# Optimization experiments

Measured on AMD Instinct MI355X. Metric: run time of the kernel, lower is better.

Reference implementation:

```python
import jax, jax.numpy as jnp
import numpy as np

N_NODES = 100000
C = 128
E = 800000
V = 50000
NEG_SLOPE = 0.2


def gat_conv(x, edges, W, att_src, att_dst, bias, num_nodes):
    """Single-head PyG-style GATConv with self-loops added (PyG default).

    edges: [2, E] with row 0 = source j, row 1 = destination i.
    """
    loops = jnp.arange(num_nodes, dtype=edges.dtype)
    src = jnp.concatenate([edges[0], loops])  # [E+N]
    dst = jnp.concatenate([edges[1], loops])

    h = x @ W.T                               # [N, C] linear transform
    a_s = h @ att_src                         # [N] per-node src score
    a_d = h @ att_dst                         # [N] per-node dst score

    e = jax.nn.leaky_relu(a_s[src] + a_d[dst], NEG_SLOPE)  # [E+N]
    # scatter-softmax over edges grouped by destination node
    m = jax.ops.segment_max(e, dst, num_segments=num_nodes)
    ex = jnp.exp(e - m[dst])
    denom = jax.ops.segment_sum(ex, dst, num_segments=num_nodes)
    alpha = ex / (denom[dst] + 1e-16)         # [E+N]

    out = jax.ops.segment_sum(alpha[:, None] * h[src], dst, num_segments=num_nodes)
    return out + bias


def setup_inputs() -> dict:
    key = jax.random.key(0)
    ks = jax.random.split(key, 12)
    s = 1.0 / np.sqrt(C)
    return {
        "embedding": jax.random.normal(ks[0], (N_NODES, C), jnp.float32),
        "W1": jax.random.normal(ks[1], (C, C), jnp.float32) * s,
        "att_src1": jax.random.normal(ks[2], (C,), jnp.float32) * s,
        "att_dst1": jax.random.normal(ks[3], (C,), jnp.float32) * s,
        "b1": jax.random.normal(ks[4], (C,), jnp.float32) * s,
        "W2": jax.random.normal(ks[5], (C, C), jnp.float32) * s,
        "att_src2": jax.random.normal(ks[6], (C,), jnp.float32) * s,
        "att_dst2": jax.random.normal(ks[7], (C,), jnp.float32) * s,
        "b2": jax.random.normal(ks[8], (C,), jnp.float32) * s,
        "edges1": jax.random.randint(ks[9], (2, E), 0, N_NODES, jnp.int64 if jax.config.jax_enable_x64 else jnp.int32),
        "edges2": jax.random.randint(ks[10], (2, E), 0, N_NODES, jnp.int64 if jax.config.jax_enable_x64 else jnp.int32),
        "idx_mapping": jax.random.randint(ks[11], (V,), 0, N_NODES, jnp.int64 if jax.config.jax_enable_x64 else jnp.int32),
    }


def reference(embedding, W1, att_src1, att_dst1, b1, W2, att_src2, att_dst2, b2,
              edges1, edges2, idx_mapping):
    h = gat_conv(embedding, edges1, W1, att_src1, att_dst1, b1, N_NODES)
    h = gat_conv(h, edges2, W2, att_src2, att_dst2, b2, N_NODES)
    return h[idx_mapping]
```

## Files before the change

kernel.cpp:

```cpp
#include <hip/hip_runtime.h>

#define N_NODES 100000
#define C_DIM 128
#define E_EDGES 800000
#define V_OUT 50000
#define EN (E_EDGES + N_NODES)
#define M2 (2 * N_NODES)
#define EN2 (2 * EN)

#define BSHIFT 9
#define NBUCK_L ((N_NODES + 511) >> 9)
#define NBUCK2 (2 * NBUCK_L)
#define CAP 8192
#define P1_CHUNK 4096
#define P1_PER_T (P1_CHUNK / 256)
#define NCHUNK ((EN2 + P1_CHUNK - 1) / P1_CHUNK)

#define XPAD 136

typedef unsigned int uint;
typedef unsigned short ushort;
typedef __attribute__((ext_vector_type(8))) short bf16x8;
typedef __attribute__((ext_vector_type(4))) float f32x4;

static __device__ __forceinline__ ushort f2bf(float f) {
    uint u = __float_as_uint(f);
    u += 0x7fffu + ((u >> 16) & 1);
    return (ushort)(u >> 16);
}

__global__ void f2bf_kernel(const float* __restrict__ in, ushort* __restrict__ out, int n4)
{
    int i = blockIdx.x * 256 + threadIdx.x;
    if (i >= n4) return;
    float4 v = reinterpret_cast<const float4*>(in)[i];
    ushort4 r;
    r.x = f2bf(v.x); r.y = f2bf(v.y); r.z = f2bf(v.z); r.w = f2bf(v.w);
    reinterpret_cast<ushort4*>(out)[i] = r;
}

__global__ void vflag_kernel(const int* __restrict__ idx, int* __restrict__ vflag)
{
    int v = blockIdx.x * 256 + threadIdx.x;
    if (v < V_OUT) vflag[idx[v]] = 1;
}

template <int IN_F32>
__global__ __launch_bounds__(256) void gemm_mfma(
    const void* __restrict__ xin, const ushort* __restrict__ Wb,
    const float* __restrict__ att_s, const float* __restrict__ att_d,
    ushort* __restrict__ hb, float* __restrict__ a_s, float* __restrict__ a_d)
{
    __shared__ ushort xs[64 * XPAD];
    __shared__ ushort ws[128 * XPAD];
    const int tid = threadIdx.x;
    const int nb = blockIdx.x * 64;

    {
        const int row = tid >> 2, q = tid & 3;
        const long srow = min(nb + row, N_NODES - 1);
        ushort* dst = &xs[row * XPAD + q * 32];
        if (IN_F32) {
            const float* src = (const float*)xin + srow * 128 + q * 32;
            #pragma unroll
            for (int i = 0; i < 4; ++i) {
                float4 u = *reinterpret_cast<const float4*>(src + i * 8);
                float4 v = *reinterpret_cast<const float4*>(src + i * 8 + 4);
                uint4 pk;
                pk.x = (uint)f2bf(u.x) | ((uint)f2bf(u.y) << 16);
                pk.y = (uint)f2bf(u.z) | ((uint)f2bf(u.w) << 16);
                pk.z = (uint)f2bf(v.x) | ((uint)f2bf(v.y) << 16);
                pk.w = (uint)f2bf(v.z) | ((uint)f2bf(v.w) << 16);
                *reinterpret_cast<uint4*>(dst + i * 8) = pk;
            }
        } else {
            const ushort* src = (const ushort*)xin + srow * 128 + q * 32;
            #pragma unroll
            for (int i = 0; i < 4; ++i)
                *reinterpret_cast<uint4*>(dst + i * 8) =
                    *reinterpret_cast<const uint4*>(src + i * 8);
        }
    }
    {
        const int row = tid >> 1, half = tid & 1;
        const ushort* src = Wb + row * 128 + half * 64;
        ushort* dst = &ws[row * XPAD + half * 64];
        #pragma unroll
        for (int i = 0; i < 8; ++i)
            *reinterpret_cast<uint4*>(dst + i * 8) =
                *reinterpret_cast<const uint4*>(src + i * 8);
    }
    __syncthreads();

    const int lane = tid & 63;
    const int wv   = tid >> 6;
    const int n0   = nb + wv * 16;
    if (n0 >= N_NODES) return;
    const int m    = lane & 15;
    const int quad = lane >> 4;

    bf16x8 a[4];
    #pragma unroll
    for (int ki = 0; ki < 4; ++ki)
        a[ki] = *reinterpret_cast<const bf16x8*>(&xs[(wv * 16 + m) * XPAD + quad * 8 + ki * 32]);

    float ps[4] = {0, 0, 0, 0}, pd[4] = {0, 0, 0, 0};

    #pragma unroll
    for (int ct = 0; ct < 8; ++ct) {
        const int c = ct * 16 + m;
        f32x4 acc = {0.f, 0.f, 0.f, 0.f};
        #pragma unroll
        for (int ki = 0; ki < 4; ++ki) {
            bf16x8 b = *reinterpret_cast<const bf16x8*>(&ws[c * XPAD + quad * 8 + ki * 32]);
            acc = __builtin_amdgcn_mfma_f32_16x16x32_bf16(a[ki], b, acc, 0, 0, 0);
        }
        const float asc = att_s[c], adc = att_d[c];
        #pragma unroll
        for (int r = 0; r < 4; ++r) {
            const int node = n0 + quad * 4 + r;
            hb[(long)node * 128 + c] = f2bf(acc[r]);
            ps[r] = fmaf(acc[r], asc, ps[r]);
            pd[r] = fmaf(acc[r], adc, pd[r]);
        }
    }
    #pragma unroll
    for (int r = 0; r < 4; ++r) {
        float s = ps[r], d = pd[r];
        #pragma unroll
        for (int x = 1; x < 16; x <<= 1) { s += __shfl_xor(s, x); d += __shfl_xor(d, x); }
        if (m == 0) {
            const int node = n0 + quad * 4 + r;
            a_s[node] = s; a_d[node] = d;
        }
    }
}

__global__ __launch_bounds__(256) void partition_kernel(
    const int* __restrict__ e1, const int* __restrict__ e2,
    int* __restrict__ cursor, uint* __restrict__ slab)
{
    __shared__ int cnt[NBUCK2];
    __shared__ int basearr[NBUCK2];
    const int tid = threadIdx.x;
    for (int i = tid; i < NBUCK2; i += 256) cnt[i] = 0;
    __syncthreads();

    const int e0 = blockIdx.x * P1_CHUNK;
    uint ent[P1_PER_T];
    int  bkt[P1_PER_T];
    #pragma unroll
    for (int i = 0; i < P1_PER_T; ++i) {
        int e = e0 + i * 256 + tid;
        bkt[i] = -1;
        if (e < EN2) {
            int src, dst, lb;
            if (e < EN) {
                if (e < E_EDGES) { src = e1[e]; dst = e1[E_EDGES + e]; }
                else             { src = dst = e - E_EDGES; }
                lb = 0;
            } else {
                int f = e - EN;
                if (f < E_EDGES) { src = e2[f]; dst = e2[E_EDGES + f]; }
                else             { src = dst = f - E_EDGES; }
                lb = NBUCK_L;
            }
            bkt[i] = lb + (dst >> BSHIFT);
            ent[i] = (uint)src | ((uint)(dst & 511) << 17);
            atomicAdd(&cnt[bkt[i]], 1);
        }
    }
    __syncthreads();
    for (int b = tid; b < NBUCK2; b += 256) {
        int c = cnt[b];
        basearr[b] = (c > 0) ? atomicAdd(&cursor[b], c) : 0;
        cnt[b] = 0;
    }
    __syncthreads();
    #pragma unroll
    for (int i = 0; i < P1_PER_T; ++i) {
        if (bkt[i] >= 0) {
            int r = basearr[bkt[i]] + atomicAdd(&cnt[bkt[i]], 1);
            if (r < CAP) slab[(long)bkt[i] * CAP + r] = ent[i];
        }
    }
}

__global__ void bucket_scan(const int* __restrict__ cursor, int* __restrict__ bbase)
{
    const int lane = threadIdx.x;
    int v[7]; int s = 0;
    #pragma unroll
    for (int i = 0; i < 7; ++i) {
        int idx = lane * 7 + i;
        v[i] = (idx < NBUCK2) ? cursor[idx] : 0;
        s += v[i];
    }
    int incl = s;
    #pragma unroll
    for (int d = 1; d < 64; d <<= 1) {
        int t = __shfl_up(incl, d);
        if (lane >= d) incl += t;
    }
    int excl = incl - s;
    #pragma unroll
    for (int i = 0; i < 7; ++i) {
        int idx = lane * 7 + i;
        if (idx < NBUCK2) bbase[idx] = excl;
        excl += v[i];
    }
}

__global__ __launch_bounds__(256) void local_csr(
    const uint* __restrict__ slab, const int* __restrict__ cursor,
    const int* __restrict__ bbase, int* __restrict__ offs, uint* __restrict__ esrc)
{
    __shared__ uint ent[CAP];
    __shared__ int deg[512];
    __shared__ int excl[512];
    const int b = blockIdx.x;
    const int tid = threadIdx.x;
    const int cnt = min(cursor[b], CAP);
    const int base = bbase[b];
    const int layer = (b >= NBUCK_L);
    const int node0 = (b - layer * NBUCK_L) << BSHIFT;
    const int obase = layer * N_NODES;
    const int nodes_n = min(512, N_NODES - node0);

    for (int i = tid; i < 512; i += 256) deg[i] = 0;
    __syncthreads();
    for (int i = tid; i < cnt; i += 256) {
        uint v = slab[(long)b * CAP + i];
        ent[i] = v;
        atomicAdd(&deg[v >> 17], 1);
    }
    __syncthreads();
    if (tid < 64) {
        int v8[8]; int s = 0;
        #pragma unroll
        for (int i = 0; i < 8; ++i) { v8[i] = deg[tid * 8 + i]; s += v8[i]; }
        int incl = s;
        #pragma unroll
        for (int d = 1; d < 64; d <<= 1) {
            int t = __shfl_up(incl, d);
            if (tid >= d) incl += t;
        }
        int e = incl - s;
        #pragma unroll
        for (int i = 0; i < 8; ++i) { excl[tid * 8 + i] = e; e += v8[i]; }
    }
    __syncthreads();
    for (int i = tid; i < nodes_n; i += 256)
        offs[obase + node0 + i] = base + excl[i];
    for (int i = tid; i < 512; i += 256) deg[i] = 0;
    if (tid == 0 && node0 + 512 >= N_NODES)
        offs[obase + N_NODES] = base + cnt;
    __syncthreads();
    for (int i = tid; i < cnt; i += 256) {
        uint v = ent[i];
        int dl = v >> 17;
        int r = atomicAdd(&deg[dl], 1);
        esrc[base + excl[dl] + r] = v;
    }
}

__global__ __launch_bounds__(256) void weights_kernel(
    const float* __restrict__ a_s, const float* __restrict__ a_d,
    const uint* __restrict__ esrc, const int* __restrict__ cursor,
    const int* __restrict__ bbase, float* __restrict__ wv, int bucket0)
{
    const int b = bucket0 + (blockIdx.x >> 2);
    const int cnt = min(cursor[b], CAP);
    const int base = bbase[b];
    const int node0 = (b - bucket0) << BSHIFT;
    for (int i = (blockIdx.x & 3) * 256 + threadIdx.x; i < cnt; i += 1024) {
        uint v = esrc[base + i];
        float e = a_s[v & 0x1ffff] + a_d[node0 + (v >> 17)];
        e = (e >= 0.0f) ? e : 0.2f * e;
        wv[base + i] = __expf(e);
    }
}

template <int MODE>
__global__ __launch_bounds__(256) void aggregate(
    const ushort* __restrict__ hb, const float* __restrict__ wv,
    const float* __restrict__ bias,
    const int* __restrict__ offs, const uint* __restrict__ esrc,
    const int* __restrict__ vflag, void* __restrict__ outp, int obase)
{
    const int wave = threadIdx.x >> 6;
    const int lane = threadIdx.x & 63;
    const int slot = lane >> 4;
    const int c16  = lane & 15;
    const int node = (blockIdx.x * 4 + wave) * 4 + slot;

    int start = offs[obase + node];
    int end   = offs[obase + node + 1];
    bool active = true;
    if (MODE == 1) { active = (vflag[node] != 0); if (!active) end = start; }

    const long coff = (long)(c16 << 3);
    float acc[8] = {0, 0, 0, 0, 0, 0, 0, 0};
    float dsum = 0.0f;

    if (start < end) {
        const int e1 = end - 1;
        uint v1 = 0; float w0, w1; uint4 h0;
        {
            uint v0 = esrc[start];
            w0 = wv[start];
            int jc = min(start + 1, e1);
            v1 = esrc[jc];
            w1 = (start + 1 < end) ? wv[jc] : 0.0f;
            h0 = *reinterpret_cast<const uint4*>(hb + ((long)(v0 & 0x1ffff) << 7) + coff);
        }
        for (int j = start; j < end; ++j) {
            const int j2 = j + 2;
            const int jc = min(j2, e1);
            uint  v2 = esrc[jc];
            float w2 = (j2 < end) ? wv[jc] : 0.0f;
            uint4 h1 = *reinterpret_cast<const uint4*>(hb + ((long)(v1 & 0x1ffff) << 7) + coff);
            dsum += w0;
            acc[0] = fmaf(w0, __uint_as_float(h0.x << 16),         acc[0]);
            acc[1] = fmaf(w0, __uint_as_float(h0.x & 0xffff0000u), acc[1]);
            acc[2] = fmaf(w0, __uint_as_float(h0.y << 16),         acc[2]);
            acc[3] = fmaf(w0, __uint_as_float(h0.y & 0xffff0000u), acc[3]);
            acc[4] = fmaf(w0, __uint_as_float(h0.z << 16),         acc[4]);
            acc[5] = fmaf(w0, __uint_as_float(h0.z & 0xffff0000u), acc[5]);
            acc[6] = fmaf(w0, __uint_as_float(h0.w << 16),         acc[6]);
            acc[7] = fmaf(w0, __uint_as_float(h0.w & 0xffff0000u), acc[7]);
            w0 = w1; h0 = h1; v1 = v2; w1 = w2;
        }
    }

    if (MODE == 1 && !active) return;

    const float inv = 1.0f / (dsum + 1e-16f);
    const int c0 = c16 << 3;
    const float4 b0 = *reinterpret_cast<const float4*>(bias + c0);
    const float4 b1 = *reinterpret_cast<const float4*>(bias + c0 + 4);
    float res[8];
    res[0] = fmaf(acc[0], inv, b0.x);
    res[1] = fmaf(acc[1], inv, b0.y);
    res[2] = fmaf(acc[2], inv, b0.z);
    res[3] = fmaf(acc[3], inv, b0.w);
    res[4] = fmaf(acc[4], inv, b1.x);
    res[5] = fmaf(acc[5], inv, b1.y);
    res[6] = fmaf(acc[6], inv, b1.z);
    res[7] = fmaf(acc[7], inv, b1.w);
    if (MODE == 0) {
        uint4 pk;
        pk.x = (uint)f2bf(res[0]) | ((uint)f2bf(res[1]) << 16);
        pk.y = (uint)f2bf(res[2]) | ((uint)f2bf(res[3]) << 16);
        pk.z = (uint)f2bf(res[4]) | ((uint)f2bf(res[5]) << 16);
        pk.w = (uint)f2bf(res[6]) | ((uint)f2bf(res[7]) << 16);
        *reinterpret_cast<uint4*>((ushort*)outp + ((long)node << 7) + c0) = pk;
    } else {
        float* op = (float*)outp + ((long)node << 7) + c0;
        *reinterpret_cast<float4*>(op)     = make_float4(res[0], res[1], res[2], res[3]);
        *reinterpret_cast<float4*>(op + 4) = make_float4(res[4], res[5], res[6], res[7]);
    }
}

__global__ void gather_out(const float* __restrict__ h, const int* __restrict__ idx,
                           float* __restrict__ out)
{
    int g = blockIdx.x * 256 + threadIdx.x;
    int v = g >> 5, c4 = (g & 31) << 2;
    long src = (long)idx[v] * C_DIM + c4;
    *reinterpret_cast<float4*>(out + ((long)v * C_DIM + c4)) =
        *reinterpret_cast<const float4*>(h + src);
}

extern "C" void kernel_launch(void* const* d_in, const int* in_sizes, int n_in,
                              void* d_out, int out_size, void* d_ws, size_t ws_size,
                              hipStream_t stream)
{
    const float* emb = (const float*)d_in[0];
    const float* W1  = (const float*)d_in[1];
    const float* as1 = (const float*)d_in[2];
    const float* ad1 = (const float*)d_in[3];
    const float* b1  = (const float*)d_in[4];
    const float* W2  = (const float*)d_in[5];
    const float* as2 = (const float*)d_in[6];
    const float* ad2 = (const float*)d_in[7];
    const float* b2  = (const float*)d_in[8];
    const int* edges1 = (const int*)d_in[9];
    const int* edges2 = (const int*)d_in[10];
    const int* idxm   = (const int*)d_in[11];
    float* out = (float*)d_out;

    char* p = (char*)d_ws;
    auto alloc = [&](size_t bytes) {
        char* r = p;
        p += (bytes + 255) & ~(size_t)255;
        return r;
    };
    float*  hB   = (float*)alloc((size_t)N_NODES * C_DIM * 4);
    ushort* hb   = (ushort*)alloc((size_t)N_NODES * C_DIM * 2);
    ushort* a1o  = (ushort*)alloc((size_t)N_NODES * C_DIM * 2);
    uint*   slab = (uint*)alloc((size_t)NBUCK2 * CAP * 4);
    uint*   esrc = (uint*)alloc((size_t)EN2 * 4);
    float*  wvb  = (float*)alloc((size_t)EN2 * 4);
    int*    offs = (int*)alloc((size_t)(M2 + 1) * 4);
    ushort* W1b  = (ushort*)alloc((size_t)C_DIM * C_DIM * 2);
    ushort* W2b  = (ushort*)alloc((size_t)C_DIM * C_DIM * 2);
    float*  aS   = (float*)alloc((size_t)N_NODES * 4);
    float*  aD   = (float*)alloc((size_t)N_NODES * 4);
    int*  bbase  = (int*)alloc((size_t)NBUCK2 * 4);
    int*  cursor = (int*)alloc((size_t)NBUCK2 * 4);
    int*  vflag  = (int*)alloc((size_t)N_NODES * 4);

    hipMemsetAsync(cursor, 0, (size_t)((char*)vflag - (char*)cursor) + (size_t)N_NODES * 4, stream);
    f2bf_kernel<<<(C_DIM * C_DIM / 4 + 255) / 256, 256, 0, stream>>>(W1, W1b, C_DIM * C_DIM / 4);
    f2bf_kernel<<<(C_DIM * C_DIM / 4 + 255) / 256, 256, 0, stream>>>(W2, W2b, C_DIM * C_DIM / 4);
    vflag_kernel<<<(V_OUT + 255) / 256, 256, 0, stream>>>(idxm, vflag);

    partition_kernel<<<NCHUNK, 256, 0, stream>>>(edges1, edges2, cursor, slab);
    bucket_scan<<<1, 64, 0, stream>>>(cursor, bbase);
    local_csr<<<NBUCK2, 256, 0, stream>>>(slab, cursor, bbase, offs, esrc);

    gemm_mfma<1><<<(N_NODES + 63) / 64, 256, 0, stream>>>(emb, W1b, as1, ad1, hb, aS, aD);
    weights_kernel<<<NBUCK_L * 4, 256, 0, stream>>>(aS, aD, esrc, cursor, bbase, wvb, 0);
    aggregate<0><<<N_NODES / 16, 256, 0, stream>>>(hb, wvb, b1, offs, esrc, vflag, a1o, 0);

    gemm_mfma<0><<<(N_NODES + 63) / 64, 256, 0, stream>>>(a1o, W2b, as2, ad2, hb, aS, aD);
    weights_kernel<<<NBUCK_L * 4, 256, 0, stream>>>(aS, aD, esrc, cursor, bbase, wvb, NBUCK_L);
    aggregate<1><<<N_NODES / 16, 256, 0, stream>>>(hb, wvb, b2, offs, esrc, vflag, hB, N_NODES);

    gather_out<<<(V_OUT * 32) / 256, 256, 0, stream>>>(hB, idxm, out);
}
```

Before: 288.2 us.

## Fuse edge weight computation into aggregation and merge prep kernels

Removes the separate weights kernel and its wv buffer. Each aggregation lane now gathers a_s[src] and a_d[node] and computes the leaky-relu exponent inline, with a deeper software pipeline so the a_s and h loads are prefetched two edges ahead. The three small prep launches (two weight conversions and the vflag marking) are merged into one kernel. This saves a full write and read of the per-edge weight array plus three launches, but every one of the 16 lanes per node now recomputes the same exp and does extra scattered a_s loads.

After: 284.1 us. Within noise of the previous version (-1.4%).

```diff
diff --git a/kernel.cpp b/kernel.cpp
--- a/kernel.cpp
+++ b/kernel.cpp
@@ -29,20 +29,25 @@
     return (ushort)(u >> 16);
 }
 
-__global__ void f2bf_kernel(const float* __restrict__ in, ushort* __restrict__ out, int n4)
-{
-    int i = blockIdx.x * 256 + threadIdx.x;
-    if (i >= n4) return;
-    float4 v = reinterpret_cast<const float4*>(in)[i];
-    ushort4 r;
-    r.x = f2bf(v.x); r.y = f2bf(v.y); r.z = f2bf(v.z); r.w = f2bf(v.w);
-    reinterpret_cast<ushort4*>(out)[i] = r;
-}
-
-__global__ void vflag_kernel(const int* __restrict__ idx, int* __restrict__ vflag)
-{
-    int v = blockIdx.x * 256 + threadIdx.x;
-    if (v < V_OUT) vflag[idx[v]] = 1;
+#define PREP_WBLK (C_DIM * C_DIM / 4 / 256)
+#define PREP_VBLK ((V_OUT + 255) / 256)
+__global__ void prep_kernel(const float* __restrict__ W1, const float* __restrict__ W2,
+                            ushort* __restrict__ W1b, ushort* __restrict__ W2b,
+                            const int* __restrict__ idx, int* __restrict__ vflag)
+{
+    const int b = blockIdx.x;
+    if (b < 2 * PREP_WBLK) {
+        const float* in  = (b < PREP_WBLK) ? W1 : W2;
+        ushort* outp     = (b < PREP_WBLK) ? W1b : W2b;
+        int i = (b % PREP_WBLK) * 256 + threadIdx.x;
+        float4 v = reinterpret_cast<const float4*>(in)[i];
+        ushort4 r;
+        r.x = f2bf(v.x); r.y = f2bf(v.y); r.z = f2bf(v.z); r.w = f2bf(v.w);
+        reinterpret_cast<ushort4*>(outp)[i] = r;
+    } else {
+        int v = (b - 2 * PREP_WBLK) * 256 + threadIdx.x;
+        if (v < V_OUT) vflag[idx[v]] = 1;
+    }
 }
 
 template <int IN_F32>
@@ -264,27 +269,10 @@
     }
 }
 
-__global__ __launch_bounds__(256) void weights_kernel(
-    const float* __restrict__ a_s, const float* __restrict__ a_d,
-    const uint* __restrict__ esrc, const int* __restrict__ cursor,
-    const int* __restrict__ bbase, float* __restrict__ wv, int bucket0)
-{
-    const int b = bucket0 + (blockIdx.x >> 2);
-    const int cnt = min(cursor[b], CAP);
-    const int base = bbase[b];
-    const int node0 = (b - bucket0) << BSHIFT;
-    for (int i = (blockIdx.x & 3) * 256 + threadIdx.x; i < cnt; i += 1024) {
-        uint v = esrc[base + i];
-        float e = a_s[v & 0x1ffff] + a_d[node0 + (v >> 17)];
-        e = (e >= 0.0f) ? e : 0.2f * e;
-        wv[base + i] = __expf(e);
-    }
-}
-
 template <int MODE>
 __global__ __launch_bounds__(256) void aggregate(
-    const ushort* __restrict__ hb, const float* __restrict__ wv,
-    const float* __restrict__ bias,
+    const ushort* __restrict__ hb, const float* __restrict__ a_s,
+    const float* __restrict__ a_d, const float* __restrict__ bias,
     const int* __restrict__ offs, const uint* __restrict__ esrc,
     const int* __restrict__ vflag, void* __restrict__ outp, int obase)
 {
@@ -304,22 +292,28 @@
     float dsum = 0.0f;
 
     if (start < end) {
+        const float ad = a_d[node];
         const int e1 = end - 1;
-        uint v1 = 0; float w0, w1; uint4 h0;
+        uint v0 = esrc[start];
+        uint v1 = esrc[min(start + 1, e1)];
+        uint v2 = esrc[min(start + 2, e1)];
+        float as1 = a_s[v1 & 0x1ffff];
+        uint4 h0 = *reinterpret_cast<const uint4*>(hb + ((long)(v0 & 0x1ffff) << 7) + coff);
+        uint4 h1 = *reinterpret_cast<const uint4*>(hb + ((long)(v1 & 0x1ffff) << 7) + coff);
+        float w0;
         {
-            uint v0 = esrc[start];
-            w0 = wv[start];
-            int jc = min(start + 1, e1);
-            v1 = esrc[jc];
-            w1 = (start + 1 < end) ? wv[jc] : 0.0f;
-            h0 = *reinterpret_cast<const uint4*>(hb + ((long)(v0 & 0x1ffff) << 7) + coff);
+            float e = a_s[v0 & 0x1ffff] + ad;
+            e = (e >= 0.0f) ? e : 0.2f * e;
+            w0 = __expf(e);
         }
         for (int j = start; j < end; ++j) {
-            const int j2 = j + 2;
-            const int jc = min(j2, e1);
-            uint  v2 = esrc[jc];
-            float w2 = (j2 < end) ? wv[jc] : 0.0f;
-            uint4 h1 = *reinterpret_cast<const uint4*>(hb + ((long)(v1 & 0x1ffff) << 7) + coff);
+            uint  v3  = esrc[min(j + 3, e1)];
+            float as2 = a_s[v2 & 0x1ffff];
+            uint4 h2  = *reinterpret_cast<const uint4*>(hb + ((long)(v2 & 0x1ffff) << 7) + coff);
+            float e   = as1 + ad;
+            e = (e >= 0.0f) ? e : 0.2f * e;
+            float w1 = __expf(e);
+
             dsum += w0;
             acc[0] = fmaf(w0, __uint_as_float(h0.x << 16),         acc[0]);
             acc[1] = fmaf(w0, __uint_as_float(h0.x & 0xffff0000u), acc[1]);
@@ -329,7 +323,7 @@
             acc[5] = fmaf(w0, __uint_as_float(h0.z & 0xffff0000u), acc[5]);
             acc[6] = fmaf(w0, __uint_as_float(h0.w << 16),         acc[6]);
             acc[7] = fmaf(w0, __uint_as_float(h0.w & 0xffff0000u), acc[7]);
-            w0 = w1; h0 = h1; v1 = v2; w1 = w2;
+            w0 = w1; h0 = h1; h1 = h2; as1 = as2; v2 = v3;
         }
     }
 
@@ -401,7 +395,6 @@
     ushort* a1o  = (ushort*)alloc((size_t)N_NODES * C_DIM * 2);
     uint*   slab = (uint*)alloc((size_t)NBUCK2 * CAP * 4);
     uint*   esrc = (uint*)alloc((size_t)EN2 * 4);
-    float*  wvb  = (float*)alloc((size_t)EN2 * 4);
     int*    offs = (int*)alloc((size_t)(M2 + 1) * 4);
     ushort* W1b  = (ushort*)alloc((size_t)C_DIM * C_DIM * 2);
     ushort* W2b  = (ushort*)alloc((size_t)C_DIM * C_DIM * 2);
@@ -412,21 +405,17 @@
     int*  vflag  = (int*)alloc((size_t)N_NODES * 4);
 
     hipMemsetAsync(cursor, 0, (size_t)((char*)vflag - (char*)cursor) + (size_t)N_NODES * 4, stream);
-    f2bf_kernel<<<(C_DIM * C_DIM / 4 + 255) / 256, 256, 0, stream>>>(W1, W1b, C_DIM * C_DIM / 4);
-    f2bf_kernel<<<(C_DIM * C_DIM / 4 + 255) / 256, 256, 0, stream>>>(W2, W2b, C_DIM * C_DIM / 4);
-    vflag_kernel<<<(V_OUT + 255) / 256, 256, 0, stream>>>(idxm, vflag);
+    prep_kernel<<<2 * PREP_WBLK + PREP_VBLK, 256, 0, stream>>>(W1, W2, W1b, W2b, idxm, vflag);
 
     partition_kernel<<<NCHUNK, 256, 0, stream>>>(edges1, edges2, cursor, slab);
     bucket_scan<<<1, 64, 0, stream>>>(cursor, bbase);
     local_csr<<<NBUCK2, 256, 0, stream>>>(slab, cursor, bbase, offs, esrc);
 
     gemm_mfma<1><<<(N_NODES + 63) / 64, 256, 0, stream>>>(emb, W1b, as1, ad1, hb, aS, aD);
-    weights_kernel<<<NBUCK_L * 4, 256, 0, stream>>>(aS, aD, esrc, cursor, bbase, wvb, 0);
-    aggregate<0><<<N_NODES / 16, 256, 0, stream>>>(hb, wvb, b1, offs, esrc, vflag, a1o, 0);
+    aggregate<0><<<N_NODES / 16, 256, 0, stream>>>(hb, aS, aD, b1, offs, esrc, vflag, a1o, 0);
 
     gemm_mfma<0><<<(N_NODES + 63) / 64, 256, 0, stream>>>(a1o, W2b, as2, ad2, hb, aS, aD);
-    weights_kernel<<<NBUCK_L * 4, 256, 0, stream>>>(aS, aD, esrc, cursor, bbase, wvb, NBUCK_L);
-    aggregate<1><<<N_NODES / 16, 256, 0, stream>>>(hb, wvb, b2, offs, esrc, vflag, hB, N_NODES);
+    aggregate<1><<<N_NODES / 16, 256, 0, stream>>>(hb, aS, aD, b2, offs, esrc, vflag, hB, N_NODES);
 
     gather_out<<<(V_OUT * 32) / 256, 256, 0, stream>>>(hB, idxm, out);
 }
```
